# Performance work log

Measured on AMD Instinct MI355X. Metric: run time of the kernel, lower is better.

## Reference

```python
import jax, jax.numpy as jnp
import numpy as np

N, T, D = 64, 2048, 256


def setup_inputs() -> dict:
    key = jax.random.key(0)
    k1, k2, k3, k4 = jax.random.split(key, 4)
    query = jax.random.normal(k1, (N, D), dtype=jnp.float32)
    key_t = jax.random.normal(k2, (N, T, D), dtype=jnp.float32)
    value = jax.random.normal(k3, (N, T, D), dtype=jnp.float32)
    lens = jax.random.randint(k4, (N,), 1, T + 1, dtype=jnp.int64)  # valid lengths in [1, T]
    return {"query": query, "key": key_t, "value": value, "lens": lens}


def reference(query, key, value, lens):
    # energy[n, t] = <key[n, t, :], query[n, :]>
    energy = jnp.einsum("ntd,nd->nt", key, query)
    attention = jax.nn.softmax(energy, axis=1)  # [N, T]
    # mask out positions >= lens[n], then renormalize over valid positions
    attention_mask = (jnp.arange(T)[None, :] < lens[:, None]).astype(attention.dtype)
    mask_attention = attention * attention_mask
    norm_attention = mask_attention / jnp.sum(mask_attention, axis=1, keepdims=True)
    # context[n, d] = sum_t norm_attention[n, t] * value[n, t, d]
    context = jnp.einsum("nt,ntd->nd", norm_attention, value)
    return (context, norm_attention)
```

## Files before the change

### kernel.cpp

```cpp
#include <hip/hip_runtime.h>


#define N_B 64
#define T_S 2048
#define D_S 256
#define TPB 256
#define RC 64
#define NC (T_S / RC)

typedef __attribute__((ext_vector_type(4))) float f4;
typedef __attribute__((ext_vector_type(2))) float f2;

__device__ __forceinline__ f4 ntload4(const float* p) {
  return __builtin_nontemporal_load((const f4*)p);
}
__device__ __forceinline__ f4 fma4(float s, f4 a, f4 b) {
  b.x = fmaf(s, a.x, b.x);
  b.y = fmaf(s, a.y, b.y);
  b.z = fmaf(s, a.z, b.z);
  b.w = fmaf(s, a.w, b.w);
  return b;
}

__global__ __launch_bounds__(TPB) void fused_kernel(
    const float* __restrict__ q, const float* __restrict__ k,
    const float* __restrict__ v, const int* __restrict__ lens,
    float* __restrict__ p_out, float2* __restrict__ mzc,
    float* __restrict__ Oc) {
  const int n = blockIdx.y, c = blockIdx.x;
  const int L = lens[n];
  const int t0 = c * RC;
  if (t0 >= L) return;
  const int tend = min(t0 + RC, L);
  const int tid = threadIdx.x;
  const int lane = tid & 63, wave = tid >> 6;

  __shared__ f4 q_sh[64];
  __shared__ float e_sh[RC];
  __shared__ float p_sh[RC];
  __shared__ f4 part[TPB];

  if (tid < 64) q_sh[tid] = ((const f4*)(q + (size_t)n * D_S))[tid];
  if (tid < RC) e_sh[tid] = -1e30f;
  __syncthreads();

  {
    const int s = lane & 15, qd = lane >> 4;
    const float* kb = k + (size_t)n * T_S * D_S + s * 4;
    const int rbase = t0 + wave * 16 + qd;
#pragma unroll
    for (int g = 0; g < 4; ++g) {
      const int r = rbase + g * 4;
      const float* krow = kb + (size_t)r * D_S;
      float acc = 0.f;
#pragma unroll
      for (int i = 0; i < 4; ++i) {
        const f4 kv = ntload4(krow + i * 64);
        const f4 qv = q_sh[i * 16 + s];
        acc = fmaf(kv.x, qv.x, acc);
        acc = fmaf(kv.y, qv.y, acc);
        acc = fmaf(kv.z, qv.z, acc);
        acc = fmaf(kv.w, qv.w, acc);
      }
#pragma unroll
      for (int off = 8; off > 0; off >>= 1) acc += __shfl_xor(acc, off, 64);
      if (s == 0 && r < tend) e_sh[r - t0] = acc;
    }
  }
  __syncthreads();

  if (wave == 0) {
    const float e = e_sh[lane];
    float m = e;
#pragma unroll
    for (int off = 32; off > 0; off >>= 1) m = fmaxf(m, __shfl_xor(m, off, 64));
    const float pv = __expf(e - m);
    float z = pv;
#pragma unroll
    for (int off = 32; off > 0; off >>= 1) z += __shfl_xor(z, off, 64);
    p_sh[lane] = pv;
    p_out[(size_t)n * T_S + t0 + lane] = pv;
    if (lane == 0) mzc[n * NC + c] = make_float2(m, z);
  }
  __syncthreads();

  const int dg = tid & 63, tg = tid >> 6;
  const float* vb = v + (size_t)n * T_S * D_S + (size_t)t0 * D_S + dg * 4;
  f4 a0 = {0.f, 0.f, 0.f, 0.f}, a1 = a0, a2 = a0, a3 = a0;
#pragma unroll
  for (int j = 0; j < 4; ++j) {
    const int r0 = j * 16 + tg;
    const f4 v0 = ntload4(vb + (size_t)r0 * D_S);
    const f4 v1 = ntload4(vb + (size_t)(r0 + 4) * D_S);
    const f4 v2 = ntload4(vb + (size_t)(r0 + 8) * D_S);
    const f4 v3 = ntload4(vb + (size_t)(r0 + 12) * D_S);
    a0 = fma4(p_sh[r0], v0, a0);
    a1 = fma4(p_sh[r0 + 4], v1, a1);
    a2 = fma4(p_sh[r0 + 8], v2, a2);
    a3 = fma4(p_sh[r0 + 12], v3, a3);
  }
  part[tid] = (a0 + a1) + (a2 + a3);
  __syncthreads();
  if (tg == 0) {
    const f4 r = part[dg] + part[dg + 64] + part[dg + 128] + part[dg + 192];
    ((f4*)(Oc + ((size_t)(n * NC + c)) * D_S))[dg] = r;
  }
}

__global__ __launch_bounds__(TPB) void merge_kernel(
    const int* __restrict__ lens, const float* __restrict__ p_in,
    const float2* __restrict__ mzc, const float* __restrict__ Oc,
    float* __restrict__ out_ctx, float* __restrict__ out_attn) {
  const int n = blockIdx.y, cx = blockIdx.x;
  const int L = lens[n];
  const int nc = (L + RC - 1) / RC;
  const int tid = threadIdx.x;
  __shared__ float s_sh[NC];
  __shared__ float cpart[TPB];

  if (tid < 64) {
    float m = -1e30f, z = 0.f;
    if (tid < nc) {
      const float2 mz = mzc[n * NC + tid];
      m = mz.x;
      z = mz.y;
    }
    float M = m;
#pragma unroll
    for (int off = 32; off > 0; off >>= 1) M = fmaxf(M, __shfl_xor(M, off, 64));
    const float sc = __expf(m - M);
    float zs = z * sc;
#pragma unroll
    for (int off = 32; off > 0; off >>= 1) zs += __shfl_xor(zs, off, 64);
    if (tid < NC) s_sh[tid] = sc / zs;
  }
  __syncthreads();

  {
    const int t = cx * (T_S / 4) + tid * 2;
    const f2 p = *(const f2*)(p_in + (size_t)n * T_S + t);
    const float sc = s_sh[t >> 6];
    f2 a;
    a.x = (t < L) ? p.x * sc : 0.f;
    a.y = (t + 1 < L) ? p.y * sc : 0.f;
    *(f2*)(out_attn + (size_t)n * T_S + t) = a;
  }

  {
    const int d = cx * 64 + (tid & 63);
    const int cg = tid >> 6;
    const float* ob = Oc + (size_t)n * NC * D_S + d;
    float acc = 0.f;
#pragma unroll
    for (int kk = 0; kk < 8; ++kk) {
      const int cc = cg + kk * 4;
      acc = fmaf(s_sh[cc], ob[(size_t)cc * D_S], acc);
    }
    cpart[tid] = acc;
    __syncthreads();
    if (tid < 64)
      out_ctx[(size_t)n * D_S + d] =
          (cpart[tid] + cpart[tid + 64]) + (cpart[tid + 128] + cpart[tid + 192]);
  }
}

extern "C" void kernel_launch(void* const* d_in, const int* in_sizes, int n_in,
                              void* d_out, int out_size, void* d_ws,
                              size_t ws_size, hipStream_t stream) {
  const float* query = (const float*)d_in[0];
  const float* key = (const float*)d_in[1];
  const float* value = (const float*)d_in[2];
  const int* lens = (const int*)d_in[3];

  float* out_ctx = (float*)d_out;
  float* out_attn = (float*)d_out + N_B * D_S;

  float* p = (float*)d_ws;
  float2* mzc = (float2*)(p + (size_t)N_B * T_S);
  float* Oc = (float*)(mzc + N_B * NC);

  const dim3 grid1(NC, N_B);
  fused_kernel<<<grid1, TPB, 0, stream>>>(query, key, value, lens, p, mzc, Oc);
  const dim3 grid2(4, N_B);
  merge_kernel<<<grid2, TPB, 0, stream>>>(lens, p, mzc, Oc, out_ctx, out_attn);
}
```

Measured before the change: 241.8 us.

## Compact fused grid to valid chunks via prefix-sum scheduling

Adds a tiny init kernel that prefix-sums per-batch chunk counts, and the fused kernel maps a flat block index to (batch, chunk) by binary search, so only valid chunks are launched densely at the front of the grid. This removes the cost of the many empty blocks that exited early and lets the real blocks be scheduled contiguously. The merge kernel also skips reading p and Oc beyond the valid length. In exchange it adds a third kernel launch and a per-block prefix load plus binary search.

```diff
diff --git a/kernel.cpp b/kernel.cpp
--- a/kernel.cpp
+++ b/kernel.cpp
@@ -7,6 +7,7 @@
 #define TPB 256
 #define RC 64
 #define NC (T_S / RC)
+#define NBLK (NC * N_B)
 
 typedef __attribute__((ext_vector_type(4))) float f4;
 typedef __attribute__((ext_vector_type(2))) float f2;
@@ -22,23 +23,46 @@
   return b;
 }
 
+__global__ void init_kernel(const int* __restrict__ lens,
+                            int* __restrict__ prefix) {
+  const int t = threadIdx.x;
+  int x = (t < N_B) ? (lens[t] + RC - 1) / RC : 0;
+#pragma unroll
+  for (int off = 1; off < 64; off <<= 1) {
+    const int y = __shfl_up(x, off, 64);
+    if (t >= off) x += y;
+  }
+  if (t < N_B) prefix[t + 1] = x;
+  if (t == 0) prefix[0] = 0;
+}
+
 __global__ __launch_bounds__(TPB) void fused_kernel(
     const float* __restrict__ q, const float* __restrict__ k,
     const float* __restrict__ v, const int* __restrict__ lens,
-    float* __restrict__ p_out, float2* __restrict__ mzc,
-    float* __restrict__ Oc) {
-  const int n = blockIdx.y, c = blockIdx.x;
-  const int L = lens[n];
-  const int t0 = c * RC;
-  if (t0 >= L) return;
-  const int tend = min(t0 + RC, L);
+    const int* __restrict__ prefix, float* __restrict__ p_out,
+    float2* __restrict__ mzc, float* __restrict__ Oc) {
   const int tid = threadIdx.x;
   const int lane = tid & 63, wave = tid >> 6;
 
+  __shared__ int P[N_B + 1];
   __shared__ f4 q_sh[64];
   __shared__ float e_sh[RC];
   __shared__ float p_sh[RC];
   __shared__ f4 part[TPB];
+
+  if (tid < N_B + 1) P[tid] = prefix[tid];
+  __syncthreads();
+  const int b = blockIdx.x;
+  if (b >= P[N_B]) return;
+  int lo = 0, hi = N_B;
+  while (hi - lo > 1) {
+    const int mid = (lo + hi) >> 1;
+    if (P[mid] <= b) lo = mid; else hi = mid;
+  }
+  const int n = lo, c = b - P[lo];
+  const int L = lens[n];
+  const int t0 = c * RC;
+  const int tend = min(t0 + RC, L);
 
   if (tid < 64) q_sh[tid] = ((const f4*)(q + (size_t)n * D_S))[tid];
   if (tid < RC) e_sh[tid] = -1e30f;
@@ -138,11 +162,13 @@
 
   {
     const int t = cx * (T_S / 4) + tid * 2;
-    const f2 p = *(const f2*)(p_in + (size_t)n * T_S + t);
-    const float sc = s_sh[t >> 6];
-    f2 a;
-    a.x = (t < L) ? p.x * sc : 0.f;
-    a.y = (t + 1 < L) ? p.y * sc : 0.f;
+    f2 a = {0.f, 0.f};
+    if (t < L) {
+      const f2 p = *(const f2*)(p_in + (size_t)n * T_S + t);
+      const float sc = s_sh[t >> 6];
+      a.x = p.x * sc;
+      a.y = (t + 1 < L) ? p.y * sc : 0.f;
+    }
     *(f2*)(out_attn + (size_t)n * T_S + t) = a;
   }
 
@@ -151,11 +177,8 @@
     const int cg = tid >> 6;
     const float* ob = Oc + (size_t)n * NC * D_S + d;
     float acc = 0.f;
-#pragma unroll
-    for (int kk = 0; kk < 8; ++kk) {
-      const int cc = cg + kk * 4;
+    for (int cc = cg; cc < nc; cc += 4)
       acc = fmaf(s_sh[cc], ob[(size_t)cc * D_S], acc);
-    }
     cpart[tid] = acc;
     __syncthreads();
     if (tid < 64)
@@ -178,9 +201,11 @@
   float* p = (float*)d_ws;
   float2* mzc = (float2*)(p + (size_t)N_B * T_S);
   float* Oc = (float*)(mzc + N_B * NC);
-
-  const dim3 grid1(NC, N_B);
-  fused_kernel<<<grid1, TPB, 0, stream>>>(query, key, value, lens, p, mzc, Oc);
+  int* prefix = (int*)(Oc + (size_t)N_B * NC * D_S);
+
+  init_kernel<<<1, 64, 0, stream>>>(lens, prefix);
+  fused_kernel<<<NBLK, TPB, 0, stream>>>(query, key, value, lens, prefix, p,
+                                         mzc, Oc);
   const dim3 grid2(4, N_B);
   merge_kernel<<<grid2, TPB, 0, stream>>>(lens, p, mzc, Oc, out_ctx, out_attn);
 }
```

New measurement: 247.1 us. +2.2%, slower.

## Merge into persistent cooperative kernel with compacted chunk list and grid syncs

Applied to the files above, without the earlier changes.

Replaces the two-kernel split with one cooperative kernel of 512 blocks that walks a prefix-sum-compacted list of only the valid 64-row chunks, so no blocks are launched for masked-out regions. The first phase computes scores and per-chunk max/sum. After a grid sync, each block applies the global softmax normalization to its chunk, writes the attention weights and accumulates value rows into per-chunk context partials. A final phase reduces the partials and zero-fills the masked attention tail. Scores stay in shared memory across the grid sync instead of going through workspace, at the cost of two grid-wide barriers and a binary search per chunk.

```diff
diff --git a/kernel.cpp b/kernel.cpp
--- a/kernel.cpp
+++ b/kernel.cpp
@@ -1,4 +1,7 @@
 #include <hip/hip_runtime.h>
+#include <hip/hip_cooperative_groups.h>
+
+namespace cg = cooperative_groups;
 
 
 #define N_B 64
@@ -7,12 +10,20 @@
 #define TPB 256
 #define RC 64
 #define NC (T_S / RC)
+#define GRID 512
+#define MAXC ((NC * N_B + GRID - 1) / GRID)
 
 typedef __attribute__((ext_vector_type(4))) float f4;
-typedef __attribute__((ext_vector_type(2))) float f2;
 
 __device__ __forceinline__ f4 ntload4(const float* p) {
   return __builtin_nontemporal_load((const f4*)p);
+}
+__device__ __forceinline__ float dot4(f4 a, f4 b, float acc) {
+  acc = fmaf(a.x, b.x, acc);
+  acc = fmaf(a.y, b.y, acc);
+  acc = fmaf(a.z, b.z, acc);
+  acc = fmaf(a.w, b.w, acc);
+  return acc;
 }
 __device__ __forceinline__ f4 fma4(float s, f4 a, f4 b) {
   b.x = fmaf(s, a.x, b.x);
@@ -22,145 +33,182 @@
   return b;
 }
 
-__global__ __launch_bounds__(TPB) void fused_kernel(
+__global__ __launch_bounds__(TPB) void mega_kernel(
     const float* __restrict__ q, const float* __restrict__ k,
     const float* __restrict__ v, const int* __restrict__ lens,
-    float* __restrict__ p_out, float2* __restrict__ mzc,
-    float* __restrict__ Oc) {
-  const int n = blockIdx.y, c = blockIdx.x;
-  const int L = lens[n];
-  const int t0 = c * RC;
-  if (t0 >= L) return;
-  const int tend = min(t0 + RC, L);
-  const int tid = threadIdx.x;
-  const int lane = tid & 63, wave = tid >> 6;
-
-  __shared__ f4 q_sh[64];
-  __shared__ float e_sh[RC];
-  __shared__ float p_sh[RC];
+    float2* __restrict__ mzc, float* __restrict__ Oc,
+    float* __restrict__ out_ctx, float* __restrict__ out_attn) {
+  const int tid = threadIdx.x, lane = tid & 63, wave = tid >> 6;
+  const int b = blockIdx.x;
+
+  __shared__ int P[N_B + 1];
+  __shared__ float e_all[MAXC][RC];
+  __shared__ float a_sh[RC];
   __shared__ f4 part[TPB];
-
-  if (tid < 64) q_sh[tid] = ((const f4*)(q + (size_t)n * D_S))[tid];
-  if (tid < RC) e_sh[tid] = -1e30f;
+  __shared__ float s_mz[2];
+
+  if (wave == 0) {
+    int x = (lens[lane] + RC - 1) >> 6;
+#pragma unroll
+    for (int off = 1; off < 64; off <<= 1) {
+      const int y = __shfl_up(x, off, 64);
+      if (lane >= off) x += y;
+    }
+    P[lane + 1] = x;
+    if (lane == 0) P[0] = 0;
+  }
   __syncthreads();
+  const int total = P[N_B];
 
   {
     const int s = lane & 15, qd = lane >> 4;
-    const float* kb = k + (size_t)n * T_S * D_S + s * 4;
-    const int rbase = t0 + wave * 16 + qd;
-#pragma unroll
-    for (int g = 0; g < 4; ++g) {
-      const int r = rbase + g * 4;
-      const float* krow = kb + (size_t)r * D_S;
-      float acc = 0.f;
-#pragma unroll
-      for (int i = 0; i < 4; ++i) {
-        const f4 kv = ntload4(krow + i * 64);
-        const f4 qv = q_sh[i * 16 + s];
-        acc = fmaf(kv.x, qv.x, acc);
-        acc = fmaf(kv.y, qv.y, acc);
-        acc = fmaf(kv.z, qv.z, acc);
-        acc = fmaf(kv.w, qv.w, acc);
-      }
-#pragma unroll
-      for (int off = 8; off > 0; off >>= 1) acc += __shfl_xor(acc, off, 64);
-      if (s == 0 && r < tend) e_sh[r - t0] = acc;
-    }
-  }
-  __syncthreads();
-
-  if (wave == 0) {
-    const float e = e_sh[lane];
-    float m = e;
-#pragma unroll
-    for (int off = 32; off > 0; off >>= 1) m = fmaxf(m, __shfl_xor(m, off, 64));
-    const float pv = __expf(e - m);
-    float z = pv;
-#pragma unroll
-    for (int off = 32; off > 0; off >>= 1) z += __shfl_xor(z, off, 64);
-    p_sh[lane] = pv;
-    p_out[(size_t)n * T_S + t0 + lane] = pv;
-    if (lane == 0) mzc[n * NC + c] = make_float2(m, z);
-  }
-  __syncthreads();
-
-  const int dg = tid & 63, tg = tid >> 6;
-  const float* vb = v + (size_t)n * T_S * D_S + (size_t)t0 * D_S + dg * 4;
-  f4 a0 = {0.f, 0.f, 0.f, 0.f}, a1 = a0, a2 = a0, a3 = a0;
-#pragma unroll
-  for (int j = 0; j < 4; ++j) {
-    const int r0 = j * 16 + tg;
-    const f4 v0 = ntload4(vb + (size_t)r0 * D_S);
-    const f4 v1 = ntload4(vb + (size_t)(r0 + 4) * D_S);
-    const f4 v2 = ntload4(vb + (size_t)(r0 + 8) * D_S);
-    const f4 v3 = ntload4(vb + (size_t)(r0 + 12) * D_S);
-    a0 = fma4(p_sh[r0], v0, a0);
-    a1 = fma4(p_sh[r0 + 4], v1, a1);
-    a2 = fma4(p_sh[r0 + 8], v2, a2);
-    a3 = fma4(p_sh[r0 + 12], v3, a3);
-  }
-  part[tid] = (a0 + a1) + (a2 + a3);
-  __syncthreads();
-  if (tg == 0) {
-    const f4 r = part[dg] + part[dg + 64] + part[dg + 128] + part[dg + 192];
-    ((f4*)(Oc + ((size_t)(n * NC + c)) * D_S))[dg] = r;
-  }
-}
-
-__global__ __launch_bounds__(TPB) void merge_kernel(
-    const int* __restrict__ lens, const float* __restrict__ p_in,
-    const float2* __restrict__ mzc, const float* __restrict__ Oc,
-    float* __restrict__ out_ctx, float* __restrict__ out_attn) {
-  const int n = blockIdx.y, cx = blockIdx.x;
-  const int L = lens[n];
-  const int nc = (L + RC - 1) / RC;
-  const int tid = threadIdx.x;
-  __shared__ float s_sh[NC];
-  __shared__ float cpart[TPB];
-
-  if (tid < 64) {
-    float m = -1e30f, z = 0.f;
-    if (tid < nc) {
-      const float2 mz = mzc[n * NC + tid];
-      m = mz.x;
-      z = mz.y;
-    }
-    float M = m;
-#pragma unroll
-    for (int off = 32; off > 0; off >>= 1) M = fmaxf(M, __shfl_xor(M, off, 64));
-    const float sc = __expf(m - M);
-    float zs = z * sc;
-#pragma unroll
-    for (int off = 32; off > 0; off >>= 1) zs += __shfl_xor(zs, off, 64);
-    if (tid < NC) s_sh[tid] = sc / zs;
-  }
-  __syncthreads();
+    int j = 0;
+    for (int ci = b; ci < total; ci += GRID, ++j) {
+      int lo = 0, hi = N_B;
+      while (hi - lo > 1) {
+        const int mid = (lo + hi) >> 1;
+        if (P[mid] <= ci) lo = mid; else hi = mid;
+      }
+      const int n = lo, c = ci - P[lo];
+      const int L = lens[n];
+      const int t0 = c * RC;
+      const int tend = min(t0 + RC, L);
+
+      if (tid < RC) e_all[j][tid] = -1e30f;
+      __syncthreads();
+
+      const float* qn = q + (size_t)n * D_S + s * 4;
+      const f4 q0 = *(const f4*)(qn);
+      const f4 q1 = *(const f4*)(qn + 64);
+      const f4 q2 = *(const f4*)(qn + 128);
+      const f4 q3 = *(const f4*)(qn + 192);
+      const float* kb =
+          k + ((size_t)n * T_S + t0 + wave * 16 + qd) * D_S + s * 4;
+#pragma unroll
+      for (int g = 0; g < 4; ++g) {
+        const float* krow = kb + (size_t)g * 4 * D_S;
+        const f4 k0 = ntload4(krow);
+        const f4 k1 = ntload4(krow + 64);
+        const f4 k2 = ntload4(krow + 128);
+        const f4 k3 = ntload4(krow + 192);
+        float acc = 0.f;
+        acc = dot4(k0, q0, acc);
+        acc = dot4(k1, q1, acc);
+        acc = dot4(k2, q2, acc);
+        acc = dot4(k3, q3, acc);
+#pragma unroll
+        for (int off = 8; off > 0; off >>= 1) acc += __shfl_xor(acc, off, 64);
+        const int r = t0 + wave * 16 + qd + g * 4;
+        if (s == 0 && r < tend) e_all[j][r - t0] = acc;
+      }
+      __syncthreads();
+      if (wave == 0) {
+        const float e = e_all[j][lane];
+        float m = e;
+#pragma unroll
+        for (int off = 32; off > 0; off >>= 1)
+          m = fmaxf(m, __shfl_xor(m, off, 64));
+        float z = __expf(e - m);
+#pragma unroll
+        for (int off = 32; off > 0; off >>= 1) z += __shfl_xor(z, off, 64);
+        if (lane == 0) mzc[n * NC + c] = make_float2(m, z);
+      }
+    }
+  }
+  __threadfence();
+  cg::this_grid().sync();
 
   {
-    const int t = cx * (T_S / 4) + tid * 2;
-    const f2 p = *(const f2*)(p_in + (size_t)n * T_S + t);
-    const float sc = s_sh[t >> 6];
-    f2 a;
-    a.x = (t < L) ? p.x * sc : 0.f;
-    a.y = (t + 1 < L) ? p.y * sc : 0.f;
-    *(f2*)(out_attn + (size_t)n * T_S + t) = a;
-  }
-
-  {
-    const int d = cx * 64 + (tid & 63);
-    const int cg = tid >> 6;
+    const int dg = tid & 63, tg = tid >> 6;
+    int j = 0;
+    for (int ci = b; ci < total; ci += GRID, ++j) {
+      int lo = 0, hi = N_B;
+      while (hi - lo > 1) {
+        const int mid = (lo + hi) >> 1;
+        if (P[mid] <= ci) lo = mid; else hi = mid;
+      }
+      const int n = lo, c = ci - P[lo];
+      const int L = lens[n];
+      const int t0 = c * RC;
+      const int nc = (L + RC - 1) >> 6;
+
+      __syncthreads();
+      if (wave == 0) {
+        float m = -1e30f, z = 0.f;
+        if (lane < nc) {
+          const float2 mz = mzc[n * NC + lane];
+          m = mz.x;
+          z = mz.y;
+        }
+        float M = m;
+#pragma unroll
+        for (int off = 32; off > 0; off >>= 1)
+          M = fmaxf(M, __shfl_xor(M, off, 64));
+        float zs = z * __expf(m - M);
+#pragma unroll
+        for (int off = 32; off > 0; off >>= 1) zs += __shfl_xor(zs, off, 64);
+        if (lane == 0) {
+          s_mz[0] = M;
+          s_mz[1] = 1.0f / zs;
+        }
+      }
+      __syncthreads();
+      if (tid < RC) {
+        const float a = __expf(e_all[j][tid] - s_mz[0]) * s_mz[1];
+        a_sh[tid] = a;
+        out_attn[(size_t)n * T_S + t0 + tid] = a;
+      }
+      __syncthreads();
+
+      const float* vb = v + ((size_t)n * T_S + t0) * D_S + dg * 4;
+      f4 a0 = {0.f, 0.f, 0.f, 0.f}, a1 = a0, a2 = a0, a3 = a0;
+#pragma unroll
+      for (int jj = 0; jj < 4; ++jj) {
+        const int r0 = jj * 16 + tg;
+        const f4 v0 = ntload4(vb + (size_t)r0 * D_S);
+        const f4 v1 = ntload4(vb + (size_t)(r0 + 4) * D_S);
+        const f4 v2 = ntload4(vb + (size_t)(r0 + 8) * D_S);
+        const f4 v3 = ntload4(vb + (size_t)(r0 + 12) * D_S);
+        a0 = fma4(a_sh[r0], v0, a0);
+        a1 = fma4(a_sh[r0 + 4], v1, a1);
+        a2 = fma4(a_sh[r0 + 8], v2, a2);
+        a3 = fma4(a_sh[r0 + 12], v3, a3);
+      }
+      part[tid] = (a0 + a1) + (a2 + a3);
+      __syncthreads();
+      if (tg == 0) {
+        const f4 r = part[dg] + part[dg + 64] + part[dg + 128] + part[dg + 192];
+        ((f4*)(Oc + (size_t)(n * NC + c) * D_S))[dg] = r;
+      }
+    }
+  }
+  __threadfence();
+  cg::this_grid().sync();
+
+  if (b < 256) {
+    const int n = b >> 2, dq = b & 3;
+    const int nc = (lens[n] + RC - 1) >> 6;
+    const int d = dq * 64 + (tid & 63);
+    const int cgi = tid >> 6;
     const float* ob = Oc + (size_t)n * NC * D_S + d;
     float acc = 0.f;
-#pragma unroll
-    for (int kk = 0; kk < 8; ++kk) {
-      const int cc = cg + kk * 4;
-      acc = fmaf(s_sh[cc], ob[(size_t)cc * D_S], acc);
-    }
-    cpart[tid] = acc;
+    for (int cc = cgi; cc < nc; cc += 4) acc += ob[(size_t)cc * D_S];
+    float* red = (float*)part;
+    red[tid] = acc;
     __syncthreads();
     if (tid < 64)
       out_ctx[(size_t)n * D_S + d] =
-          (cpart[tid] + cpart[tid + 64]) + (cpart[tid + 128] + cpart[tid + 192]);
+          (red[tid] + red[tid + 64]) + (red[tid + 128] + red[tid + 192]);
+  } else {
+    const int b2 = b - 256;
+    const int n = b2 >> 2, qr = b2 & 3;
+    const int start0 = ((lens[n] + RC - 1) >> 6) << 6;
+    const int base = qr * (T_S / 4);
+#pragma unroll
+    for (int i = 0; i < 2; ++i) {
+      const int t = base + i * TPB + tid;
+      if (t >= start0) out_attn[(size_t)n * T_S + t] = 0.f;
+    }
   }
 }
 
@@ -175,12 +223,12 @@
   float* out_ctx = (float*)d_out;
   float* out_attn = (float*)d_out + N_B * D_S;
 
-  float* p = (float*)d_ws;
-  float2* mzc = (float2*)(p + (size_t)N_B * T_S);
-  float* Oc = (float*)(mzc + N_B * NC);
-
-  const dim3 grid1(NC, N_B);
-  fused_kernel<<<grid1, TPB, 0, stream>>>(query, key, value, lens, p, mzc, Oc);
-  const dim3 grid2(4, N_B);
-  merge_kernel<<<grid2, TPB, 0, stream>>>(lens, p, mzc, Oc, out_ctx, out_attn);
-}
+  float2* mzc = (float2*)d_ws;
+  float* Oc = (float*)d_ws + 2 * (size_t)N_B * NC;
+
+  void* args[8] = {(void*)&query, (void*)&key,   (void*)&value,
+                   (void*)&lens,  (void*)&mzc,   (void*)&Oc,
+                   (void*)&out_ctx, (void*)&out_attn};
+  hipLaunchCooperativeKernel((const void*)mega_kernel, dim3(GRID), dim3(TPB),
+                             args, 0, stream);
+}
```

New measurement: 507.6 us. 2.1x slower.

## Prefetch V tile into registers before QK dot product and trim merge work

Applied to the files above, without the earlier changes.

The fused kernel now issues all V loads for its chunk into a 16-entry register array at kernel start, so they overlap with the K loads, dot products and softmax instead of waiting behind them. Q is read directly into registers rather than staged through shared memory, which removes one barrier. The launch bounds now request 3 blocks per CU. The merge kernel skips reading attention values past the valid length and loops only over valid chunks instead of all 32. The register prefetch raises VGPR pressure, which may limit occupancy or cause spills.

```diff
diff --git a/kernel.cpp b/kernel.cpp
--- a/kernel.cpp
+++ b/kernel.cpp
@@ -14,6 +14,13 @@
 __device__ __forceinline__ f4 ntload4(const float* p) {
   return __builtin_nontemporal_load((const f4*)p);
 }
+__device__ __forceinline__ float dot4(f4 a, f4 b, float acc) {
+  acc = fmaf(a.x, b.x, acc);
+  acc = fmaf(a.y, b.y, acc);
+  acc = fmaf(a.z, b.z, acc);
+  acc = fmaf(a.w, b.w, acc);
+  return acc;
+}
 __device__ __forceinline__ f4 fma4(float s, f4 a, f4 b) {
   b.x = fmaf(s, a.x, b.x);
   b.y = fmaf(s, a.y, b.y);
@@ -22,7 +29,7 @@
   return b;
 }
 
-__global__ __launch_bounds__(TPB) void fused_kernel(
+__global__ __launch_bounds__(TPB, 3) void fused_kernel(
     const float* __restrict__ q, const float* __restrict__ k,
     const float* __restrict__ v, const int* __restrict__ lens,
     float* __restrict__ p_out, float2* __restrict__ mzc,
@@ -35,36 +42,46 @@
   const int tid = threadIdx.x;
   const int lane = tid & 63, wave = tid >> 6;
 
-  __shared__ f4 q_sh[64];
   __shared__ float e_sh[RC];
   __shared__ float p_sh[RC];
   __shared__ f4 part[TPB];
 
-  if (tid < 64) q_sh[tid] = ((const f4*)(q + (size_t)n * D_S))[tid];
-  if (tid < RC) e_sh[tid] = -1e30f;
-  __syncthreads();
+  const int dg = tid & 63, tg = tid >> 6;
+  const float* vb = v + ((size_t)n * T_S + t0) * D_S + dg * 4;
+  f4 vreg[16];
+#pragma unroll
+  for (int j = 0; j < 4; ++j) {
+    const int r0 = j * 16 + tg;
+    vreg[j * 4 + 0] = ntload4(vb + (size_t)r0 * D_S);
+    vreg[j * 4 + 1] = ntload4(vb + (size_t)(r0 + 4) * D_S);
+    vreg[j * 4 + 2] = ntload4(vb + (size_t)(r0 + 8) * D_S);
+    vreg[j * 4 + 3] = ntload4(vb + (size_t)(r0 + 12) * D_S);
+  }
 
   {
     const int s = lane & 15, qd = lane >> 4;
-    const float* kb = k + (size_t)n * T_S * D_S + s * 4;
-    const int rbase = t0 + wave * 16 + qd;
+    const float* qn = q + (size_t)n * D_S + s * 4;
+    const f4 q0 = *(const f4*)(qn);
+    const f4 q1 = *(const f4*)(qn + 64);
+    const f4 q2 = *(const f4*)(qn + 128);
+    const f4 q3 = *(const f4*)(qn + 192);
+    const float* kb = k + ((size_t)n * T_S + t0 + wave * 16 + qd) * D_S + s * 4;
 #pragma unroll
     for (int g = 0; g < 4; ++g) {
-      const int r = rbase + g * 4;
-      const float* krow = kb + (size_t)r * D_S;
+      const float* krow = kb + (size_t)g * 4 * D_S;
+      const f4 k0 = ntload4(krow);
+      const f4 k1 = ntload4(krow + 64);
+      const f4 k2 = ntload4(krow + 128);
+      const f4 k3 = ntload4(krow + 192);
       float acc = 0.f;
-#pragma unroll
-      for (int i = 0; i < 4; ++i) {
-        const f4 kv = ntload4(krow + i * 64);
-        const f4 qv = q_sh[i * 16 + s];
-        acc = fmaf(kv.x, qv.x, acc);
-        acc = fmaf(kv.y, qv.y, acc);
-        acc = fmaf(kv.z, qv.z, acc);
-        acc = fmaf(kv.w, qv.w, acc);
-      }
+      acc = dot4(k0, q0, acc);
+      acc = dot4(k1, q1, acc);
+      acc = dot4(k2, q2, acc);
+      acc = dot4(k3, q3, acc);
 #pragma unroll
       for (int off = 8; off > 0; off >>= 1) acc += __shfl_xor(acc, off, 64);
-      if (s == 0 && r < tend) e_sh[r - t0] = acc;
+      const int r = t0 + wave * 16 + qd + g * 4;
+      if (s == 0) e_sh[r - t0] = (r < tend) ? acc : -1e30f;
     }
   }
   __syncthreads();
@@ -84,20 +101,14 @@
   }
   __syncthreads();
 
-  const int dg = tid & 63, tg = tid >> 6;
-  const float* vb = v + (size_t)n * T_S * D_S + (size_t)t0 * D_S + dg * 4;
   f4 a0 = {0.f, 0.f, 0.f, 0.f}, a1 = a0, a2 = a0, a3 = a0;
 #pragma unroll
   for (int j = 0; j < 4; ++j) {
     const int r0 = j * 16 + tg;
-    const f4 v0 = ntload4(vb + (size_t)r0 * D_S);
-    const f4 v1 = ntload4(vb + (size_t)(r0 + 4) * D_S);
-    const f4 v2 = ntload4(vb + (size_t)(r0 + 8) * D_S);
-    const f4 v3 = ntload4(vb + (size_t)(r0 + 12) * D_S);
-    a0 = fma4(p_sh[r0], v0, a0);
-    a1 = fma4(p_sh[r0 + 4], v1, a1);
-    a2 = fma4(p_sh[r0 + 8], v2, a2);
-    a3 = fma4(p_sh[r0 + 12], v3, a3);
+    a0 = fma4(p_sh[r0], vreg[j * 4 + 0], a0);
+    a1 = fma4(p_sh[r0 + 4], vreg[j * 4 + 1], a1);
+    a2 = fma4(p_sh[r0 + 8], vreg[j * 4 + 2], a2);
+    a3 = fma4(p_sh[r0 + 12], vreg[j * 4 + 3], a3);
   }
   part[tid] = (a0 + a1) + (a2 + a3);
   __syncthreads();
@@ -113,7 +124,7 @@
     float* __restrict__ out_ctx, float* __restrict__ out_attn) {
   const int n = blockIdx.y, cx = blockIdx.x;
   const int L = lens[n];
-  const int nc = (L + RC - 1) / RC;
+  const int nc = (L + RC - 1) >> 6;
   const int tid = threadIdx.x;
   __shared__ float s_sh[NC];
   __shared__ float cpart[TPB];
@@ -138,11 +149,13 @@
 
   {
     const int t = cx * (T_S / 4) + tid * 2;
-    const f2 p = *(const f2*)(p_in + (size_t)n * T_S + t);
-    const float sc = s_sh[t >> 6];
-    f2 a;
-    a.x = (t < L) ? p.x * sc : 0.f;
-    a.y = (t + 1 < L) ? p.y * sc : 0.f;
+    f2 a = {0.f, 0.f};
+    if (t < L) {
+      const f2 p = *(const f2*)(p_in + (size_t)n * T_S + t);
+      const float sc = s_sh[t >> 6];
+      a.x = p.x * sc;
+      a.y = (t + 1 < L) ? p.y * sc : 0.f;
+    }
     *(f2*)(out_attn + (size_t)n * T_S + t) = a;
   }
 
@@ -151,11 +164,8 @@
     const int cg = tid >> 6;
     const float* ob = Oc + (size_t)n * NC * D_S + d;
     float acc = 0.f;
-#pragma unroll
-    for (int kk = 0; kk < 8; ++kk) {
-      const int cc = cg + kk * 4;
+    for (int cc = cg; cc < nc; cc += 4)
       acc = fmaf(s_sh[cc], ob[(size_t)cc * D_S], acc);
-    }
     cpart[tid] = acc;
     __syncthreads();
     if (tid < 64)
```

Result: no change. 245.5 us (+1.5%).
